# Performance work log

Measured on AMD Instinct MI355X. Metric: run time of the kernel, lower is better.

The kernel has to match this reference:

```python
import jax, jax.numpy as jnp
import numpy as np

B, T, C, H = 2, 2048, 1024, 16
HD = C // H  # head_dim = 64


def setup_inputs() -> dict:
    key = jax.random.key(0)
    ks = jax.random.split(key, 5)
    x = jax.random.normal(ks[0], (B, T, C), dtype=jnp.float32)
    # realistic rotary tables: cos/sin of position*inv_freq, shape (T, HD//2)
    inv_freq = 1.0 / (10000.0 ** (jnp.arange(0, HD, 2, dtype=jnp.float32) / HD))
    ang = jnp.arange(T, dtype=jnp.float32)[:, None] * inv_freq[None, :]
    cos, sin = jnp.cos(ang), jnp.sin(ang)
    w_attn = jax.random.normal(ks[1], (C, 3 * C), dtype=jnp.float32) * (C ** -0.5)
    b_attn = jnp.zeros((3 * C,), dtype=jnp.float32)
    w_proj = jax.random.normal(ks[2], (C, C), dtype=jnp.float32) * (C ** -0.5)
    b_proj = jnp.zeros((C,), dtype=jnp.float32)
    return {"x": x, "cos": cos, "sin": sin, "w_attn": w_attn, "b_attn": b_attn,
            "w_proj": w_proj, "b_proj": b_proj}


def _apply_rotary(x, cos, sin):
    # x: (B, H, T, HD); cos/sin: (T, HD//2) broadcast over B,H
    x_even = x[..., ::2]
    x_odd = x[..., 1::2]
    rot = jnp.stack((x_even * cos - x_odd * sin, x_even * sin + x_odd * cos), axis=-1)
    return rot.reshape(*x.shape[:-1], x.shape[-1])


def reference(x, cos, sin, w_attn, b_attn, w_proj, b_proj):
    b, t, c = x.shape
    qkv = x @ w_attn + b_attn                       # (B, T, 3C)
    q, k, v = jnp.split(qkv, 3, axis=-1)
    # (B, T, C) -> (B, H, T, HD)
    def to_heads(z):
        return z.reshape(b, t, H, HD).transpose(0, 2, 1, 3)
    q, k, v = to_heads(q), to_heads(k), to_heads(v)
    q = _apply_rotary(q, cos, sin)
    k = _apply_rotary(k, cos, sin)
    scale = 1.0 / jnp.sqrt(jnp.asarray(HD, dtype=x.dtype))
    scores = jnp.einsum('bhqd,bhkd->bhqk', q, k) * scale
    causal = jnp.tril(jnp.ones((t, t), dtype=bool))
    scores = jnp.where(causal, scores, jnp.asarray(-jnp.inf, dtype=scores.dtype))
    attn = jax.nn.softmax(scores, axis=-1)
    y = jnp.einsum('bhqk,bhkd->bhqd', attn, v)      # (B, H, T, HD)
    y = y.transpose(0, 2, 1, 3).reshape(b, t, c)
    return y @ w_proj + b_proj
```

## Files before the change

kernel.cpp:

```cpp
#include <hip/hip_runtime.h>
#include <hip/hip_bf16.h>
#include <math.h>

#define Bsz 2
#define Tseq 2048
#define Cdim 1024
#define Hn 16
#define HDim 64
#define Mrows 4096
#define N3 3072
#define QSCALE 0.1803368801111137f

typedef __bf16 bf16_t;
typedef __bf16 bf16x4 __attribute__((ext_vector_type(4)));
typedef __bf16 bf16x8 __attribute__((ext_vector_type(8)));
typedef float floatx4 __attribute__((ext_vector_type(4)));

__device__ __forceinline__ void async16(const void* g, void* l) {
    __builtin_amdgcn_global_load_lds(
        (const __attribute__((address_space(1))) void*)g,
        (__attribute__((address_space(3))) void*)l, 16, 0, 0);
}

__global__ __launch_bounds__(256) void prep_kernel(
    const float* __restrict__ x, const float* __restrict__ w_attn,
    const float* __restrict__ w_proj, bf16_t* __restrict__ xb,
    bf16_t* __restrict__ waT, bf16_t* __restrict__ wpT)
{
    __shared__ float Ts[32][33];
    const int bid = blockIdx.x;
    if (bid < 2048) {
        size_t g = (size_t)bid * 256 + threadIdx.x;
        float4 a = *(const float4*)(x + g * 8);
        float4 b = *(const float4*)(x + g * 8 + 4);
        bf16x8 o;
        o[0] = (bf16_t)a.x; o[1] = (bf16_t)a.y; o[2] = (bf16_t)a.z; o[3] = (bf16_t)a.w;
        o[4] = (bf16_t)b.x; o[5] = (bf16_t)b.y; o[6] = (bf16_t)b.z; o[7] = (bf16_t)b.w;
        *(bf16x8*)(xb + g * 8) = o;
        return;
    }
    const float* in; bf16_t* out; int R, C, bx, by;
    if (bid < 5120) {
        int t = bid - 2048; in = w_attn; out = waT; R = Cdim; C = N3;
        bx = t % 96; by = t / 96;
    } else {
        int t = bid - 5120; in = w_proj; out = wpT; R = Cdim; C = Cdim;
        bx = t & 31; by = t >> 5;
    }
    int c0 = bx << 5, r0 = by << 5;
    int lr = threadIdx.x >> 3, lc = (threadIdx.x & 7) << 2;
    float4 v = *(const float4*)(in + (size_t)(r0 + lr) * C + c0 + lc);
    Ts[lr][lc] = v.x; Ts[lr][lc + 1] = v.y; Ts[lr][lc + 2] = v.z; Ts[lr][lc + 3] = v.w;
    __syncthreads();
    bf16x4 o;
    o[0] = (bf16_t)Ts[lc + 0][lr]; o[1] = (bf16_t)Ts[lc + 1][lr];
    o[2] = (bf16_t)Ts[lc + 2][lr]; o[3] = (bf16_t)Ts[lc + 3][lr];
    *(bf16x4*)(out + (size_t)(c0 + lr) * R + r0 + lc) = o;
}

__global__ __launch_bounds__(256) void gemm_qkv(
    const bf16_t* __restrict__ xb, const bf16_t* __restrict__ waT,
    const float* __restrict__ bias, const float* __restrict__ cosb,
    const float* __restrict__ sinb,
    bf16_t* __restrict__ qb, bf16_t* __restrict__ kb, bf16_t* __restrict__ vt)
{
    __shared__ bf16_t As[128 * 32];
    __shared__ bf16_t Bs[128 * 32];
    const int tid = threadIdx.x;
    const int lane = tid & 63, w = tid >> 6;
    const int lm = lane & 15, quad = lane >> 4;
    const int wy = w >> 1, wx = w & 1;
    const int bid = blockIdx.x;
    const int xcd = bid & 7, i5 = bid >> 3;
    const int gn = ((xcd & 1) * 12) + (i5 % 12);
    const int gm = ((xcd >> 1) * 8) + (i5 / 12);
    const int m0 = gm << 7, n0 = gn << 7;

    const floatx4 fz = {0.f, 0.f, 0.f, 0.f};
    floatx4 acc[4][4];
    #pragma unroll
    for (int i = 0; i < 4; i++)
        #pragma unroll
        for (int j = 0; j < 4; j++) acc[i][j] = fz;

    const bf16_t* Ag = xb + (size_t)m0 * Cdim;
    const bf16_t* Bg = waT + (size_t)n0 * Cdim;

    for (int k0 = 0; k0 < Cdim; k0 += 32) {
        #pragma unroll
        for (int it = 0; it < 2; ++it) {
            int ci = (w << 7) + (it << 6) + lane;
            int row = ci >> 2, cq = (ci & 3) ^ (row & 3);
            async16(Ag + (size_t)row * Cdim + k0 + cq * 8, As + ((w << 7) + (it << 6)) * 8);
            async16(Bg + (size_t)row * Cdim + k0 + cq * 8, Bs + ((w << 7) + (it << 6)) * 8);
        }
        __syncthreads();
        bf16x8 af[4], bfr[4];
        #pragma unroll
        for (int i = 0; i < 4; i++) {
            int row = (wy << 6) + (i << 4) + lm;
            int cq = quad ^ (lm & 3);
            af[i] = *(const bf16x8*)&As[row * 32 + cq * 8];
        }
        #pragma unroll
        for (int j = 0; j < 4; j++) {
            int row = (wx << 6) + (j << 4) + lm;
            int cq = quad ^ (lm & 3);
            bfr[j] = *(const bf16x8*)&Bs[row * 32 + cq * 8];
        }
        #pragma unroll
        for (int i = 0; i < 4; i++)
            #pragma unroll
            for (int j = 0; j < 4; j++)
                acc[i][j] = __builtin_amdgcn_mfma_f32_16x16x32_bf16(af[i], bfr[j], acc[i][j], 0, 0, 0);
        __syncthreads();
    }

    const int sec = n0 >> 10;
    const int mb = m0 + (wy << 6);
    const int nb = n0 + (wx << 6);
    #pragma unroll
    for (int i = 0; i < 4; i++) {
        int mrow0 = mb + (i << 4) + (quad << 2);
        int b = mrow0 >> 11, t0 = mrow0 & 2047;
        #pragma unroll
        for (int j = 0; j < 4; j++) {
            int n = nb + (j << 4) + lm;
            float bi = bias[n];
            int rel = n & 1023;
            int h = rel >> 6, hd = rel & 63;
            if (sec == 2) {
                int tp = (t0 & ~31) | (((t0 >> 2) & 3) << 3) | (((t0 >> 4) & 1) << 2);
                bf16x4 pk;
                #pragma unroll
                for (int r = 0; r < 4; r++) pk[r] = (bf16_t)(acc[i][j][r] + bi);
                *(bf16x4*)&vt[((size_t)(b * Hn + h) * HDim + hd) * Tseq + tp] = pk;
            } else {
                bf16_t* dst = (sec == 0) ? qb : kb;
                const int ih = hd >> 1;
                const bool ev = !(hd & 1);
                #pragma unroll
                for (int r = 0; r < 4; r++) {
                    int t = t0 + r;
                    float v = acc[i][j][r] + bi;
                    float x = __shfl_xor(v, 1);
                    float c = cosb[t * 32 + ih], s = sinb[t * 32 + ih];
                    float rv = ev ? (v * c - x * s) : (x * s + v * c);
                    if (sec == 0) rv *= QSCALE;
                    dst[((size_t)(b * Hn + h) * Tseq + t) * HDim + hd] = (bf16_t)rv;
                }
            }
        }
    }
}

__global__ __launch_bounds__(256) void attn_mfma(
    const bf16_t* __restrict__ qb, const bf16_t* __restrict__ kb,
    const bf16_t* __restrict__ vt, bf16_t* __restrict__ yb)
{
    __shared__ bf16_t Ks[2][64 * 64];
    __shared__ bf16_t VTs[2][64 * 64];

    const int bid = blockIdx.x;
    const int jt = 31 - (bid >> 5);
    const int bh = bid & 31;
    const int b = bh >> 4, h = bh & 15;
    const int tid = threadIdx.x;
    const int w4 = tid >> 6, lane = tid & 63, lm = lane & 15, quad = lane >> 4;
    const int nk = jt + 1;

    {
        const bf16_t* Kg = kb + (size_t)bh * Tseq * HDim;
        const bf16_t* Vg = vt + (size_t)bh * HDim * Tseq;
        #pragma unroll
        for (int it = 0; it < 2; ++it) {
            int ci = (it << 8) + tid;
            int row = ci >> 3, cq = (ci & 7) ^ (row & 7);
            async16(Kg + row * HDim + cq * 8, &Ks[0][((it << 8) + (w4 << 6)) * 8]);
            async16(Vg + (size_t)row * Tseq + cq * 8, &VTs[0][((it << 8) + (w4 << 6)) * 8]);
        }
    }

    const int qq = (jt << 6) + (w4 << 4) + lm;
    bf16x8 qf[2];
    {
        const bf16_t* Qg = qb + ((size_t)bh * Tseq + qq) * HDim;
        #pragma unroll
        for (int ks = 0; ks < 2; ++ks)
            qf[ks] = *(const bf16x8*)(Qg + (ks << 5) + (quad << 3));
    }
    __syncthreads();

    const floatx4 fz = {0.f, 0.f, 0.f, 0.f};
    floatx4 o_[4];
    #pragma unroll
    for (int f = 0; f < 4; ++f) o_[f] = fz;
    float l_ = 0.f;

    for (int kt = 0; kt < nk; ++kt) {
        const int cb = kt & 1;
        if (kt + 1 < nk) {
            const int nb2 = cb ^ 1;
            const bf16_t* Kg = kb + ((size_t)bh * Tseq + ((kt + 1) << 6)) * HDim;
            const bf16_t* Vg = vt + (size_t)bh * HDim * Tseq + ((kt + 1) << 6);
            #pragma unroll
            for (int it = 0; it < 2; ++it) {
                int ci = (it << 8) + tid;
                int row = ci >> 3, cq = (ci & 7) ^ (row & 7);
                async16(Kg + row * HDim + cq * 8, &Ks[nb2][((it << 8) + (w4 << 6)) * 8]);
                async16(Vg + (size_t)row * Tseq + cq * 8, &VTs[nb2][((it << 8) + (w4 << 6)) * 8]);
            }
        }

        floatx4 st[4];
        #pragma unroll
        for (int sub = 0; sub < 4; ++sub) st[sub] = fz;
        #pragma unroll
        for (int ks = 0; ks < 2; ++ks) {
            bf16x8 kf[4];
            #pragma unroll
            for (int sub = 0; sub < 4; ++sub) {
                int krow = (sub << 4) + lm;
                int kc = ((ks << 2) + quad) ^ (krow & 7);
                kf[sub] = *(const bf16x8*)&Ks[cb][krow * 64 + kc * 8];
            }
            #pragma unroll
            for (int sub = 0; sub < 4; ++sub)
                st[sub] = __builtin_amdgcn_mfma_f32_16x16x32_bf16(
                    kf[sub], qf[ks], st[sub], 0, 0, 0);
        }

        const bool dm = (kt == jt);
        bf16x8 pf[2];
        float rs = 0.f;
        #pragma unroll
        for (int cc = 0; cc < 2; ++cc)
            #pragma unroll
            for (int jj = 0; jj < 8; ++jj) {
                int sub = (cc << 1) + (jj >> 2), r = jj & 3;
                float val = st[sub][r];
                if (dm) {
                    int key = (kt << 6) + (sub << 4) + (quad << 2) + r;
                    if (key > qq) val = -3e38f;
                }
                float p = exp2f(val);
                rs += p;
                pf[cc][jj] = (bf16_t)p;
            }
        rs += __shfl_xor(rs, 16);
        rs += __shfl_xor(rs, 32);
        l_ += rs;

        #pragma unroll
        for (int cc = 0; cc < 2; ++cc) {
            bf16x8 vf[4];
            #pragma unroll
            for (int f = 0; f < 4; ++f) {
                int vrow = (f << 4) + lm;
                int vc = ((cc << 2) + quad) ^ (vrow & 7);
                vf[f] = *(const bf16x8*)&VTs[cb][vrow * 64 + vc * 8];
            }
            #pragma unroll
            for (int f = 0; f < 4; ++f)
                o_[f] = __builtin_amdgcn_mfma_f32_16x16x32_bf16(
                    vf[f], pf[cc], o_[f], 0, 0, 0);
        }
        __syncthreads();
    }

    {
        float inv = 1.f / l_;
        size_t base = ((size_t)(b * Tseq) + qq) * Cdim + (h << 6) + (quad << 2);
        #pragma unroll
        for (int f = 0; f < 4; ++f) {
            bf16x4 ov;
            #pragma unroll
            for (int r = 0; r < 4; ++r) ov[r] = (bf16_t)(o_[f][r] * inv);
            *(bf16x4*)&yb[base + (f << 4)] = ov;
        }
    }
}

__global__ __launch_bounds__(256) void gemm_proj(
    const bf16_t* __restrict__ yb, const bf16_t* __restrict__ wpT,
    const float* __restrict__ bias, float* __restrict__ out)
{
    __shared__ bf16_t As[128 * 32];
    __shared__ bf16_t Bs[128 * 32];
    const int tid = threadIdx.x;
    const int lane = tid & 63, w = tid >> 6;
    const int lm = lane & 15, quad = lane >> 4;
    const int wy = w >> 1, wx = w & 1;
    const int bid = blockIdx.x;
    const int xcd = bid & 7, i5 = bid >> 3;
    const int gn = i5 & 7;
    const int gm = (xcd << 2) + (i5 >> 3);
    const int m0 = gm << 7, n0 = gn << 7;

    const floatx4 fz = {0.f, 0.f, 0.f, 0.f};
    floatx4 acc[4][4];
    #pragma unroll
    for (int i = 0; i < 4; i++)
        #pragma unroll
        for (int j = 0; j < 4; j++) acc[i][j] = fz;

    const bf16_t* Ag = yb + (size_t)m0 * Cdim;
    const bf16_t* Bg = wpT + (size_t)n0 * Cdim;

    for (int k0 = 0; k0 < Cdim; k0 += 32) {
        #pragma unroll
        for (int it = 0; it < 2; ++it) {
            int ci = (w << 7) + (it << 6) + lane;
            int row = ci >> 2, cq = (ci & 3) ^ (row & 3);
            async16(Ag + (size_t)row * Cdim + k0 + cq * 8, As + ((w << 7) + (it << 6)) * 8);
            async16(Bg + (size_t)row * Cdim + k0 + cq * 8, Bs + ((w << 7) + (it << 6)) * 8);
        }
        __syncthreads();
        bf16x8 af[4], bfr[4];
        #pragma unroll
        for (int i = 0; i < 4; i++) {
            int row = (wy << 6) + (i << 4) + lm;
            int cq = quad ^ (lm & 3);
            af[i] = *(const bf16x8*)&As[row * 32 + cq * 8];
        }
        #pragma unroll
        for (int j = 0; j < 4; j++) {
            int row = (wx << 6) + (j << 4) + lm;
            int cq = quad ^ (lm & 3);
            bfr[j] = *(const bf16x8*)&Bs[row * 32 + cq * 8];
        }
        #pragma unroll
        for (int i = 0; i < 4; i++)
            #pragma unroll
            for (int j = 0; j < 4; j++)
                acc[i][j] = __builtin_amdgcn_mfma_f32_16x16x32_bf16(af[i], bfr[j], acc[i][j], 0, 0, 0);
        __syncthreads();
    }

    const int mb = m0 + (wy << 6);
    const int nb = n0 + (wx << 6);
    #pragma unroll
    for (int i = 0; i < 4; i++) {
        int mrow0 = mb + (i << 4) + (quad << 2);
        #pragma unroll
        for (int j = 0; j < 4; j++) {
            int n = nb + (j << 4) + lm;
            float bi = bias[n];
            #pragma unroll
            for (int r = 0; r < 4; r++)
                out[(size_t)(mrow0 + r) * Cdim + n] = acc[i][j][r] + bi;
        }
    }
}

extern "C" void kernel_launch(void* const* d_in, const int* in_sizes, int n_in,
                              void* d_out, int out_size, void* d_ws, size_t ws_size,
                              hipStream_t stream) {
    const float* x      = (const float*)d_in[0];
    const float* cosb   = (const float*)d_in[1];
    const float* sinb   = (const float*)d_in[2];
    const float* w_attn = (const float*)d_in[3];
    const float* b_attn = (const float*)d_in[4];
    const float* w_proj = (const float*)d_in[5];
    const float* b_proj = (const float*)d_in[6];

    char* ws = (char*)d_ws;
    bf16_t* xb  = (bf16_t*)(ws);
    bf16_t* waT = (bf16_t*)(ws + (size_t)(8 << 20));
    bf16_t* wpT = (bf16_t*)(ws + (size_t)(14 << 20));
    bf16_t* qb  = (bf16_t*)(ws + (size_t)(16 << 20));
    bf16_t* kb  = (bf16_t*)(ws + (size_t)(24 << 20));
    bf16_t* vtb = (bf16_t*)(ws + (size_t)(32 << 20));
    bf16_t* yb  = (bf16_t*)(ws + (size_t)(40 << 20));

    prep_kernel<<<6144, 256, 0, stream>>>(x, w_attn, w_proj, xb, waT, wpT);
    gemm_qkv<<<768, 256, 0, stream>>>(xb, waT, b_attn, cosb, sinb, qb, kb, vtb);
    attn_mfma<<<1024, 256, 0, stream>>>(qb, kb, vtb, yb);
    gemm_proj<<<256, 256, 0, stream>>>(yb, wpT, b_proj, (float*)d_out);
}
```

Before: 185.1 us.

## Rewrite QKV GEMM as 256x256 tile with multi-stage async LDS pipeline

The QKV projection GEMM now uses 256x256 output tiles with 512 threads (8 waves, 2x4 layout, 8x4 MFMA accumulators per wave) instead of 128x128 tiles with 4 waves. The main loop is a 4-stage ping-pong pipeline: global-to-LDS async loads for future K slices are issued inside each compute phase and gated by vmcnt waits and raw barriers, with setprio around the MFMA bursts and a new LDS swizzle. This is meant to hide load latency and raise arithmetic intensity per block. The cost is a 192-block grid that fills the CUs less evenly, plus higher register pressure and LDS use (128KB).

Measured after the change: 191.6 us. 1.04x slower.

```diff
diff --git a/kernel.cpp b/kernel.cpp
--- a/kernel.cpp
+++ b/kernel.cpp
@@ -58,69 +58,98 @@
     *(bf16x4*)(out + (size_t)(c0 + lr) * R + r0 + lc) = o;
 }
 
-__global__ __launch_bounds__(256) void gemm_qkv(
+#define VMW(N) asm volatile("s_waitcnt vmcnt(" #N ")" ::: "memory")
+
+#define STAGE(HALF, SRC, KOFF) do {                                          \
+    _Pragma("unroll") for (int _it = 0; _it < 2; ++_it) {                    \
+        int _ci = (_it << 9) + tid;                                          \
+        int _r = _ci >> 2, _sl = _ci & 3;                                    \
+        int _cg = _sl ^ ((_r >> 1) & 3);                                     \
+        async16((SRC) + (size_t)_r * Cdim + (KOFF) + _cg * 8,                \
+                (HALF) + ((_it << 9) + (w << 6)) * 8);                       \
+    } } while (0)
+
+#define PHASE(AARR, BARR, S, RH, ...) do {                                   \
+    bf16x8 _af[4], _bf[4];                                                   \
+    _Pragma("unroll") for (int _f = 0; _f < 4; ++_f) {                       \
+        int _ra = (wy << 7) + ((RH) << 6) + (_f << 4) + lm;                  \
+        _af[_f] = *(const bf16x8*)&AARR[S][(_ra * 4 + (quad ^ ((_ra >> 1) & 3))) * 8]; \
+        int _rb = (wx << 6) + (_f << 4) + lm;                                \
+        _bf[_f] = *(const bf16x8*)&BARR[S][(_rb * 4 + (quad ^ ((_rb >> 1) & 3))) * 8]; \
+    }                                                                        \
+    __VA_ARGS__;                                                             \
+    __builtin_amdgcn_s_barrier();                                            \
+    __builtin_amdgcn_s_setprio(1);                                           \
+    _Pragma("unroll") for (int _f = 0; _f < 4; ++_f)                         \
+        _Pragma("unroll") for (int _j = 0; _j < 4; ++_j)                     \
+            acc[((RH) << 2) + _f][_j] = __builtin_amdgcn_mfma_f32_16x16x32_bf16( \
+                _af[_f], _bf[_j], acc[((RH) << 2) + _f][_j], 0, 0, 0);       \
+    __builtin_amdgcn_s_setprio(0);                                           \
+    __builtin_amdgcn_s_barrier();                                            \
+} while (0)
+
+__global__ __launch_bounds__(512) void gemm_qkv(
     const bf16_t* __restrict__ xb, const bf16_t* __restrict__ waT,
     const float* __restrict__ bias, const float* __restrict__ cosb,
     const float* __restrict__ sinb,
     bf16_t* __restrict__ qb, bf16_t* __restrict__ kb, bf16_t* __restrict__ vt)
 {
-    __shared__ bf16_t As[128 * 32];
-    __shared__ bf16_t Bs[128 * 32];
+    __shared__ bf16_t A0[2][8192];
+    __shared__ bf16_t B0[2][8192];
+    __shared__ bf16_t A1[2][8192];
+    __shared__ bf16_t B1[2][8192];
+
     const int tid = threadIdx.x;
     const int lane = tid & 63, w = tid >> 6;
     const int lm = lane & 15, quad = lane >> 4;
-    const int wy = w >> 1, wx = w & 1;
+    const int wy = w >> 2, wx = w & 3;
     const int bid = blockIdx.x;
-    const int xcd = bid & 7, i5 = bid >> 3;
-    const int gn = ((xcd & 1) * 12) + (i5 % 12);
-    const int gm = ((xcd >> 1) * 8) + (i5 / 12);
-    const int m0 = gm << 7, n0 = gn << 7;
+    const int xcd = bid & 7, idx = bid >> 3;
+    const int gn = (xcd & 1) * 6 + idx % 6;
+    const int gm = (xcd >> 1) * 4 + idx / 6;
+    const int m0 = gm << 8, n0 = gn << 8;
 
     const floatx4 fz = {0.f, 0.f, 0.f, 0.f};
-    floatx4 acc[4][4];
+    floatx4 acc[8][4];
     #pragma unroll
-    for (int i = 0; i < 4; i++)
+    for (int i = 0; i < 8; i++)
         #pragma unroll
         for (int j = 0; j < 4; j++) acc[i][j] = fz;
 
     const bf16_t* Ag = xb + (size_t)m0 * Cdim;
     const bf16_t* Bg = waT + (size_t)n0 * Cdim;
 
-    for (int k0 = 0; k0 < Cdim; k0 += 32) {
-        #pragma unroll
-        for (int it = 0; it < 2; ++it) {
-            int ci = (w << 7) + (it << 6) + lane;
-            int row = ci >> 2, cq = (ci & 3) ^ (row & 3);
-            async16(Ag + (size_t)row * Cdim + k0 + cq * 8, As + ((w << 7) + (it << 6)) * 8);
-            async16(Bg + (size_t)row * Cdim + k0 + cq * 8, Bs + ((w << 7) + (it << 6)) * 8);
-        }
-        __syncthreads();
-        bf16x8 af[4], bfr[4];
-        #pragma unroll
-        for (int i = 0; i < 4; i++) {
-            int row = (wy << 6) + (i << 4) + lm;
-            int cq = quad ^ (lm & 3);
-            af[i] = *(const bf16x8*)&As[row * 32 + cq * 8];
-        }
-        #pragma unroll
-        for (int j = 0; j < 4; j++) {
-            int row = (wx << 6) + (j << 4) + lm;
-            int cq = quad ^ (lm & 3);
-            bfr[j] = *(const bf16x8*)&Bs[row * 32 + cq * 8];
-        }
-        #pragma unroll
-        for (int i = 0; i < 4; i++)
-            #pragma unroll
-            for (int j = 0; j < 4; j++)
-                acc[i][j] = __builtin_amdgcn_mfma_f32_16x16x32_bf16(af[i], bfr[j], acc[i][j], 0, 0, 0);
-        __syncthreads();
-    }
+    STAGE(A0[0], Ag, 0);  STAGE(B0[0], Bg, 0);
+    STAGE(A0[1], Ag, 32); STAGE(B0[1], Bg, 32);
+    STAGE(A1[0], Ag, 64); STAGE(B1[0], Bg, 64);
+    VMW(8);
+    __builtin_amdgcn_s_barrier();
+
+    for (int t2 = 0; t2 < 7; ++t2) {
+        const int kE = t2 << 7;
+        VMW(4); PHASE(A0, B0, 0, 0, STAGE(A1[1], Ag, kE + 96));
+                PHASE(A0, B0, 0, 1, STAGE(B1[1], Bg, kE + 96));
+        VMW(4); PHASE(A0, B0, 1, 0, STAGE(A0[0], Ag, kE + 128));
+                PHASE(A0, B0, 1, 1, STAGE(B0[0], Bg, kE + 128));
+        VMW(4); PHASE(A1, B1, 0, 0, STAGE(A0[1], Ag, kE + 160));
+                PHASE(A1, B1, 0, 1, STAGE(B0[1], Bg, kE + 160));
+        VMW(4); PHASE(A1, B1, 1, 0, STAGE(A1[0], Ag, kE + 192));
+                PHASE(A1, B1, 1, 1, STAGE(B1[0], Bg, kE + 192));
+    }
+    VMW(4); PHASE(A0, B0, 0, 0, STAGE(A1[1], Ag, 992));
+            PHASE(A0, B0, 0, 1, STAGE(B1[1], Bg, 992));
+    VMW(4); PHASE(A0, B0, 1, 0, ((void)0));
+            PHASE(A0, B0, 1, 1, ((void)0));
+    VMW(0); PHASE(A1, B1, 0, 0, ((void)0));
+            PHASE(A1, B1, 0, 1, ((void)0));
+            PHASE(A1, B1, 1, 0, ((void)0));
+            PHASE(A1, B1, 1, 1, ((void)0));
 
     const int sec = n0 >> 10;
-    const int mb = m0 + (wy << 6);
+    const int mb = m0 + (wy << 7);
     const int nb = n0 + (wx << 6);
     #pragma unroll
-    for (int i = 0; i < 4; i++) {
+    for (int i = 0; i < 8; i++) {
         int mrow0 = mb + (i << 4) + (quad << 2);
         int b = mrow0 >> 11, t0 = mrow0 & 2047;
         #pragma unroll
@@ -374,7 +403,7 @@
     bf16_t* yb  = (bf16_t*)(ws + (size_t)(40 << 20));
 
     prep_kernel<<<6144, 256, 0, stream>>>(x, w_attn, w_proj, xb, waT, wpT);
-    gemm_qkv<<<768, 256, 0, stream>>>(xb, waT, b_attn, cosb, sinb, qb, kb, vtb);
+    gemm_qkv<<<192, 512, 0, stream>>>(xb, waT, b_attn, cosb, sinb, qb, kb, vtb);
     attn_mfma<<<1024, 256, 0, stream>>>(qb, kb, vtb, yb);
     gemm_proj<<<256, 256, 0, stream>>>(yb, wpT, b_proj, (float*)d_out);
 }
```
